# Performance work log

Hardware: AMD Instinct MI355X
Metric: run time of the kernel (lower is better)

## Reference

```python
import jax, jax.numpy as jnp
import numpy as np

DROPOUT = 0.5
ALPHA = 0.15
N_PROPAGATION = 5


def setup_inputs() -> dict:
    key = jax.random.key(0)
    k1, k2, k3, k4 = jax.random.split(key, 4)
    n_nodes, n_edges, d = 100000, 1600000, 48
    logits = jax.random.normal(k1, (n_nodes, d), dtype=jnp.float32)
    edge_val = jax.random.uniform(k2, (n_edges,), dtype=jnp.float32)
    edge_row = jax.random.randint(k3, (n_edges,), 0, n_nodes, dtype=jnp.int32)
    edge_col = jax.random.randint(k4, (n_edges,), 0, n_nodes, dtype=jnp.int32)
    return {"logits": logits, "edge_val": edge_val,
            "edge_row": edge_row, "edge_col": edge_col}


def reference(logits, edge_val, edge_row, edge_col):
    # APPNP-style power iteration: x <- (1-alpha) * dropout(A_hat) @ x + alpha * logits
    n_nodes = logits.shape[0]
    keep = 1.0 - DROPOUT
    drop_key = jax.random.key(42)
    a = logits
    x = logits
    for i in range(N_PROPAGATION):
        ki = jax.random.fold_in(drop_key, i)
        mask = jax.random.bernoulli(ki, keep, edge_val.shape)
        vals = jnp.where(mask, edge_val * (1.0 / keep), 0.0)  # inverted dropout on nnz values
        msg = vals[:, None] * x[edge_col]                      # [E, d] gather + scale
        spmm = jax.ops.segment_sum(msg, edge_row, num_segments=n_nodes)  # [N, d]
        x = (1.0 - ALPHA) * spmm + ALPHA * a
    return x
```

## Files before the change

### kernel.cpp

```cpp
#include <hip/hip_runtime.h>
#include <stdint.h>
#include <stddef.h>

#define D 48
#define BLK 256
#define BLKA 1024
#define EPTA 4
#define CHUNK (BLKA * EPTA)
#define BLD 512
#define BSH 9
#define NBKT_MAX 256
#define B97 0x30800000u

struct U2 { uint32_t a, b; };

__host__ __device__ constexpr U2 tf2x32(uint32_t k0, uint32_t k1, uint32_t c0, uint32_t c1) {
  uint32_t ks2 = k0 ^ k1 ^ 0x1BD11BDAu;
  uint32_t x0 = c0 + k0, x1 = c1 + k1;
#define TFR(r) x0 += x1; x1 = (x1 << (r)) | (x1 >> (32 - (r))); x1 ^= x0;
  TFR(13) TFR(15) TFR(26) TFR(6)
  x0 += k1; x1 += ks2 + 1u;
  TFR(17) TFR(29) TFR(16) TFR(24)
  x0 += ks2; x1 += k0 + 2u;
  TFR(13) TFR(15) TFR(26) TFR(6)
  x0 += k0; x1 += k1 + 3u;
  TFR(17) TFR(29) TFR(16) TFR(24)
  x0 += k1; x1 += ks2 + 4u;
  TFR(13) TFR(15) TFR(26) TFR(6)
  x0 += ks2; x1 += k0 + 5u;
#undef TFR
  return U2{x0, x1};
}

struct __align__(8) Edge { uint32_t cm; float val; };

__global__ __launch_bounds__(BLKA) void k_bkt_hist(
    const int* __restrict__ erow, int* __restrict__ bkt, int E, int nbkt) {
  __shared__ int h[NBKT_MAX];
  int t = threadIdx.x;
  int j0 = blockIdx.x * CHUNK;
  for (int i = t; i < nbkt; i += BLKA) h[i] = 0;
  __syncthreads();
#pragma unroll
  for (int k = 0; k < EPTA; ++k) {
    int j = j0 + k * BLKA + t;
    if (j < E) atomicAdd(&h[erow[j] >> BSH], 1);
  }
  __syncthreads();
  for (int i = t; i < nbkt; i += BLKA)
    if (h[i]) atomicAdd(&bkt[i], h[i]);
}

__global__ __launch_bounds__(BLK) void k_scan_bkt(
    int* __restrict__ bkt, int* __restrict__ bcur, int nbkt, int E) {
  __shared__ int s[BLK];
  int t = threadIdx.x;
  int v = (t < nbkt) ? bkt[t] : 0;
  s[t] = v;
  __syncthreads();
  for (int off = 1; off < BLK; off <<= 1) {
    int u = (t >= off) ? s[t - off] : 0;
    __syncthreads();
    s[t] += u;
    __syncthreads();
  }
  if (t < nbkt) {
    int excl = s[t] - v;
    bkt[t]  = excl;
    bcur[t] = excl;
  }
  if (t == 0) bkt[nbkt] = E;
}

__global__ __launch_bounds__(BLKA) void k_bucket_ms(
    const int* __restrict__ erow, const int* __restrict__ ecol,
    const float* __restrict__ eval,
    int* __restrict__ bcur, int* __restrict__ segcnt,
    Edge* __restrict__ es_b, int* __restrict__ rowb, int E, int nbkt) {
  __shared__ int h[NBKT_MAX];
  __shared__ int base[NBKT_MAX];
  __shared__ int hk[5][NBKT_MAX];
  constexpr U2 K0 = tf2x32(0u, 42u, 0u, 0u);
  constexpr U2 K1 = tf2x32(0u, 42u, 0u, 1u);
  constexpr U2 K2 = tf2x32(0u, 42u, 0u, 2u);
  constexpr U2 K3 = tf2x32(0u, 42u, 0u, 3u);
  constexpr U2 K4 = tf2x32(0u, 42u, 0u, 4u);
  int t = threadIdx.x;
  int j0 = blockIdx.x * CHUNK;
  for (int i = t; i < nbkt; i += BLKA) {
    h[i] = 0;
    for (int q = 0; q < 5; ++q) hk[q][i] = 0;
  }
  __syncthreads();
#pragma unroll
  for (int k = 0; k < EPTA; ++k) {
    int j = j0 + k * BLKA + t;
    if (j < E) atomicAdd(&h[erow[j] >> BSH], 1);
  }
  __syncthreads();
  for (int i = t; i < nbkt; i += BLKA)
    base[i] = h[i] ? atomicAdd(&bcur[i], h[i]) : 0;
  __syncthreads();
  for (int i = t; i < nbkt; i += BLKA) h[i] = 0;
  __syncthreads();
#pragma unroll
  for (int k = 0; k < EPTA; ++k) {
    int j = j0 + k * BLKA + t;
    if (j >= E) continue;
    int row = erow[j];
    int b = row >> BSH;
    uint32_t uj = (uint32_t)j;
    unsigned m = 0;
    U2 r;
    r = tf2x32(K0.a, K0.b, 0u, uj); m |= ((((r.a ^ r.b) >> 31) ^ 1u) << 0);
    r = tf2x32(K1.a, K1.b, 0u, uj); m |= ((((r.a ^ r.b) >> 31) ^ 1u) << 1);
    r = tf2x32(K2.a, K2.b, 0u, uj); m |= ((((r.a ^ r.b) >> 31) ^ 1u) << 2);
    r = tf2x32(K3.a, K3.b, 0u, uj); m |= ((((r.a ^ r.b) >> 31) ^ 1u) << 3);
    r = tf2x32(K4.a, K4.b, 0u, uj); m |= ((((r.a ^ r.b) >> 31) ^ 1u) << 4);
#pragma unroll
    for (int q = 0; q < 5; ++q)
      if ((m >> q) & 1u) atomicAdd(&hk[q][b], 1);
    int slot = atomicAdd(&h[b], 1);
    int p = base[b] + slot;
    Edge eg;
    eg.cm  = (uint32_t)ecol[j] | (m << 20);
    eg.val = eval[j] * 2.0f;
    es_b[p] = eg;
    rowb[p] = row;
  }
  __syncthreads();
  for (int i = t; i < nbkt; i += BLKA)
    for (int q = 0; q < 5; ++q)
      if (hk[q][i]) atomicAdd(&segcnt[q * nbkt + i], hk[q][i]);
}

__global__ __launch_bounds__(1024) void k_scan_seg(
    int* __restrict__ seg, int* __restrict__ rp5, int nbkt, int N) {
  __shared__ int s[1024];
  int t = threadIdx.x;
  int n = 5 * nbkt;
  int v = (t < n) ? seg[t] : 0;
  s[t] = v;
  __syncthreads();
  for (int off = 1; off < 1024; off <<= 1) {
    int u = (t >= off) ? s[t - off] : 0;
    __syncthreads();
    s[t] += u;
    __syncthreads();
  }
  if (t <= n) seg[t] = s[t] - v;
  __syncthreads();
  if (t < 5) rp5[(size_t)t * (N + 1) + N] = seg[(t + 1) * nbkt];
}

__global__ __launch_bounds__(BLD) void k_build(
    const Edge* __restrict__ es_b, const int* __restrict__ rowb,
    const int* __restrict__ bkt_off, const int* __restrict__ segoff,
    int* __restrict__ rp5, uint32_t* __restrict__ es_all, int N, int nbkt) {
  __shared__ int lc[5][1 << BSH];
  __shared__ int sc[1 << BSH];
  int b = blockIdx.x, t = threadIdx.x;
  int s = bkt_off[b], e = bkt_off[b + 1];
  int rbase = b << BSH;
#pragma unroll
  for (int i = 0; i < 5; ++i) lc[i][t] = 0;
  __syncthreads();
  for (int j = s + t; j < e; j += BLD) {
    int row = rowb[j] - rbase;
    unsigned m = es_b[j].cm >> 20;
#pragma unroll
    for (int i = 0; i < 5; ++i)
      if ((m >> i) & 1u) atomicAdd(&lc[i][row], 1);
  }
  __syncthreads();
  for (int i = 0; i < 5; ++i) {
    int v = lc[i][t];
    sc[t] = v;
    __syncthreads();
    for (int off = 1; off < BLD; off <<= 1) {
      int u = (t >= off) ? sc[t - off] : 0;
      __syncthreads();
      sc[t] += u;
      __syncthreads();
    }
    int pos = segoff[i * nbkt + b] + sc[t] - v;
    int row = rbase + t;
    if (row < N) rp5[(size_t)i * (N + 1) + row] = pos;
    lc[i][t] = pos;
    __syncthreads();
  }
  for (int j = s + t; j < e; j += BLD) {
    int row = rowb[j] - rbase;
    Edge eg = es_b[j];
    unsigned m = eg.cm >> 20;
    uint32_t vb = __float_as_uint(eg.val);
    uint32_t pk = (vb < B97) ? 0u : ((vb - B97 + (1u << 12)) >> 13);
    uint32_t entry = (eg.cm & 0x1FFFFu) | (pk << 17);
#pragma unroll
    for (int i = 0; i < 5; ++i)
      if ((m >> i) & 1u) {
        int p = atomicAdd(&lc[i][row], 1);
        es_all[p] = entry;
      }
  }
}

__global__ __launch_bounds__(BLK) void k_spmm(
    const int* __restrict__ rp, const uint32_t* __restrict__ es_all,
    const float* __restrict__ x, const float* __restrict__ logits,
    float* __restrict__ xn, int N) {
  int t = blockIdx.x * BLK + threadIdx.x;
  int r = t >> 4;
  if (r >= N) return;
  int sl = t & 15;
  int s = rp[r], e = rp[r + 1];
  float a0 = 0.f, a1 = 0.f, a2 = 0.f;
  const float* xb = x + 3 * sl;
  for (int k = s; k < e; k += 8) {
#pragma unroll
    for (int i = 0; i < 8; ++i) {
      int kk = k + i;
      bool in = kk < e;
      uint32_t u = es_all[kk];
      int c = in ? (int)(u & 0x1FFFFu) : 0;
      uint32_t vb = ((u >> 17) << 13) + B97;
      float v = in ? __uint_as_float(vb) : 0.0f;
      const float* xp = xb + (size_t)c * D;
      a0 = fmaf(v, xp[0], a0);
      a1 = fmaf(v, xp[1], a1);
      a2 = fmaf(v, xp[2], a2);
    }
  }
  size_t o = (size_t)r * D + 3 * sl;
  xn[o + 0] = 0.85f * a0 + 0.15f * logits[o + 0];
  xn[o + 1] = 0.85f * a1 + 0.15f * logits[o + 1];
  xn[o + 2] = 0.85f * a2 + 0.15f * logits[o + 2];
}

extern "C" void kernel_launch(void* const* d_in, const int* in_sizes, int n_in,
                              void* d_out, int out_size, void* d_ws, size_t ws_size,
                              hipStream_t stream) {
  const float* logits   = (const float*)d_in[0];
  const float* edge_val = (const float*)d_in[1];
  const int*   edge_row = (const int*)d_in[2];
  const int*   edge_col = (const int*)d_in[3];
  float* out = (float*)d_out;

  const int E = in_sizes[1];
  const int N = in_sizes[0] / D;
  const int EBC  = (E + CHUNK - 1) / CHUNK;
  const int NBKT = (N + (1 << BSH) - 1) >> BSH;

  char* p = (char*)d_ws;
  auto alloc = [&](size_t bytes) {
    char* q = p;
    p += (bytes + 255) & ~(size_t)255;
    return q;
  };
  int* rp5     = (int*)alloc((size_t)5 * (N + 1) * 4);
  int* bkt     = (int*)alloc((size_t)(NBKT + 1) * 4);
  int* bcur    = (int*)alloc((size_t)NBKT * 4);
  int* segcnt  = (int*)alloc((size_t)(5 * NBKT + 1) * 4);
  uint32_t* es_all = (uint32_t*)alloc(((size_t)E * 5 / 2 + 65536) * 4);
  size_t un_sz = (size_t)E * 12 + 512;
  size_t xa_sz = (size_t)N * D * 4;
  char* un = alloc(un_sz > xa_sz ? un_sz : xa_sz);
  Edge* es_b = (Edge*)un;
  int*  rowb = (int*)(un + (((size_t)E * 8 + 255) & ~(size_t)255));
  float* xA  = (float*)un;

  hipMemsetAsync(bkt, 0, (size_t)(NBKT + 1) * 4, stream);
  hipMemsetAsync(segcnt, 0, (size_t)(5 * NBKT + 1) * 4, stream);
  k_bkt_hist<<<EBC, BLKA, 0, stream>>>(edge_row, bkt, E, NBKT);
  k_scan_bkt<<<1, BLK, 0, stream>>>(bkt, bcur, NBKT, E);
  k_bucket_ms<<<EBC, BLKA, 0, stream>>>(edge_row, edge_col, edge_val,
                                        bcur, segcnt, es_b, rowb, E, NBKT);
  k_scan_seg<<<1, 1024, 0, stream>>>(segcnt, rp5, NBKT, N);
  k_build<<<NBKT, BLD, 0, stream>>>(es_b, rowb, bkt, segcnt, rp5, es_all, N, NBKT);

  const int RPB = BLK / 16;
  const float* src = logits;
  float* dst = out;
  for (int i = 0; i < 5; ++i) {
    k_spmm<<<(N + RPB - 1) / RPB, BLK, 0, stream>>>(rp5 + (size_t)i * (N + 1),
                                                    es_all, src, logits, dst, N);
    src = dst;
    dst = (dst == out) ? xA : out;
  }
}
```

Baseline: 330.9 us.

## Store propagated features and logits in bf16, halve lanes per row

The node feature matrix and logits are converted to bf16 with round-to-nearest-even. Each SpMM iteration then gathers packed bf16 pairs, accumulates in fp32 with 8 lanes per row handling 6 features each, and writes bf16 except on the final pass, which writes fp32. This halves the gather and store traffic in the propagation loop. Separately, the per-iteration dropout count histogram moves into the first histogram pass, so the bucketing kernel no longer does those atomics. The cost is bf16 rounding error compounded over five iterations, plus the mask being computed twice across the two passes.

```diff
diff --git a/kernel.cpp b/kernel.cpp
--- a/kernel.cpp
+++ b/kernel.cpp
@@ -32,23 +32,70 @@
   return U2{x0, x1};
 }
 
+__device__ __forceinline__ unsigned mask5_of(uint32_t uj) {
+  constexpr U2 K0 = tf2x32(0u, 42u, 0u, 0u);
+  constexpr U2 K1 = tf2x32(0u, 42u, 0u, 1u);
+  constexpr U2 K2 = tf2x32(0u, 42u, 0u, 2u);
+  constexpr U2 K3 = tf2x32(0u, 42u, 0u, 3u);
+  constexpr U2 K4 = tf2x32(0u, 42u, 0u, 4u);
+  unsigned m = 0;
+  U2 r;
+  r = tf2x32(K0.a, K0.b, 0u, uj); m |= ((((r.a ^ r.b) >> 31) ^ 1u) << 0);
+  r = tf2x32(K1.a, K1.b, 0u, uj); m |= ((((r.a ^ r.b) >> 31) ^ 1u) << 1);
+  r = tf2x32(K2.a, K2.b, 0u, uj); m |= ((((r.a ^ r.b) >> 31) ^ 1u) << 2);
+  r = tf2x32(K3.a, K3.b, 0u, uj); m |= ((((r.a ^ r.b) >> 31) ^ 1u) << 3);
+  r = tf2x32(K4.a, K4.b, 0u, uj); m |= ((((r.a ^ r.b) >> 31) ^ 1u) << 4);
+  return m;
+}
+
+__device__ __forceinline__ uint32_t rne16(float f) {
+  uint32_t u = __float_as_uint(f);
+  return (u + 0x7FFFu + ((u >> 16) & 1u)) >> 16;
+}
+__device__ __forceinline__ uint32_t pk2(float a, float b) {
+  return rne16(a) | (rne16(b) << 16);
+}
+
 struct __align__(8) Edge { uint32_t cm; float val; };
 
+__global__ __launch_bounds__(BLK) void k_prep(
+    const float4* __restrict__ in, uint2* __restrict__ outp, int n4) {
+  int i = blockIdx.x * BLK + threadIdx.x;
+  if (i >= n4) return;
+  float4 f = in[i];
+  outp[i] = make_uint2(pk2(f.x, f.y), pk2(f.z, f.w));
+}
+
 __global__ __launch_bounds__(BLKA) void k_bkt_hist(
-    const int* __restrict__ erow, int* __restrict__ bkt, int E, int nbkt) {
+    const int* __restrict__ erow, int* __restrict__ bkt,
+    int* __restrict__ segcnt, int E, int nbkt) {
   __shared__ int h[NBKT_MAX];
+  __shared__ int hk[5][NBKT_MAX + 1];
   int t = threadIdx.x;
   int j0 = blockIdx.x * CHUNK;
-  for (int i = t; i < nbkt; i += BLKA) h[i] = 0;
+  for (int i = t; i < nbkt; i += BLKA) {
+    h[i] = 0;
+    for (int q = 0; q < 5; ++q) hk[q][i] = 0;
+  }
   __syncthreads();
 #pragma unroll
   for (int k = 0; k < EPTA; ++k) {
     int j = j0 + k * BLKA + t;
-    if (j < E) atomicAdd(&h[erow[j] >> BSH], 1);
-  }
-  __syncthreads();
-  for (int i = t; i < nbkt; i += BLKA)
+    if (j < E) {
+      int b = erow[j] >> BSH;
+      atomicAdd(&h[b], 1);
+      unsigned m = mask5_of((uint32_t)j);
+#pragma unroll
+      for (int q = 0; q < 5; ++q)
+        if ((m >> q) & 1u) atomicAdd(&hk[q][b], 1);
+    }
+  }
+  __syncthreads();
+  for (int i = t; i < nbkt; i += BLKA) {
     if (h[i]) atomicAdd(&bkt[i], h[i]);
+    for (int q = 0; q < 5; ++q)
+      if (hk[q][i]) atomicAdd(&segcnt[q * nbkt + i], hk[q][i]);
+  }
 }
 
 __global__ __launch_bounds__(BLK) void k_scan_bkt(
@@ -75,22 +122,13 @@
 __global__ __launch_bounds__(BLKA) void k_bucket_ms(
     const int* __restrict__ erow, const int* __restrict__ ecol,
     const float* __restrict__ eval,
-    int* __restrict__ bcur, int* __restrict__ segcnt,
-    Edge* __restrict__ es_b, int* __restrict__ rowb, int E, int nbkt) {
+    int* __restrict__ bcur, Edge* __restrict__ es_b, int* __restrict__ rowb,
+    int E, int nbkt) {
   __shared__ int h[NBKT_MAX];
   __shared__ int base[NBKT_MAX];
-  __shared__ int hk[5][NBKT_MAX];
-  constexpr U2 K0 = tf2x32(0u, 42u, 0u, 0u);
-  constexpr U2 K1 = tf2x32(0u, 42u, 0u, 1u);
-  constexpr U2 K2 = tf2x32(0u, 42u, 0u, 2u);
-  constexpr U2 K3 = tf2x32(0u, 42u, 0u, 3u);
-  constexpr U2 K4 = tf2x32(0u, 42u, 0u, 4u);
   int t = threadIdx.x;
   int j0 = blockIdx.x * CHUNK;
-  for (int i = t; i < nbkt; i += BLKA) {
-    h[i] = 0;
-    for (int q = 0; q < 5; ++q) hk[q][i] = 0;
-  }
+  for (int i = t; i < nbkt; i += BLKA) h[i] = 0;
   __syncthreads();
 #pragma unroll
   for (int k = 0; k < EPTA; ++k) {
@@ -109,17 +147,7 @@
     if (j >= E) continue;
     int row = erow[j];
     int b = row >> BSH;
-    uint32_t uj = (uint32_t)j;
-    unsigned m = 0;
-    U2 r;
-    r = tf2x32(K0.a, K0.b, 0u, uj); m |= ((((r.a ^ r.b) >> 31) ^ 1u) << 0);
-    r = tf2x32(K1.a, K1.b, 0u, uj); m |= ((((r.a ^ r.b) >> 31) ^ 1u) << 1);
-    r = tf2x32(K2.a, K2.b, 0u, uj); m |= ((((r.a ^ r.b) >> 31) ^ 1u) << 2);
-    r = tf2x32(K3.a, K3.b, 0u, uj); m |= ((((r.a ^ r.b) >> 31) ^ 1u) << 3);
-    r = tf2x32(K4.a, K4.b, 0u, uj); m |= ((((r.a ^ r.b) >> 31) ^ 1u) << 4);
-#pragma unroll
-    for (int q = 0; q < 5; ++q)
-      if ((m >> q) & 1u) atomicAdd(&hk[q][b], 1);
+    unsigned m = mask5_of((uint32_t)j);
     int slot = atomicAdd(&h[b], 1);
     int p = base[b] + slot;
     Edge eg;
@@ -128,10 +156,6 @@
     es_b[p] = eg;
     rowb[p] = row;
   }
-  __syncthreads();
-  for (int i = t; i < nbkt; i += BLKA)
-    for (int q = 0; q < 5; ++q)
-      if (hk[q][i]) atomicAdd(&segcnt[q * nbkt + i], hk[q][i]);
 }
 
 __global__ __launch_bounds__(1024) void k_scan_seg(
@@ -205,17 +229,18 @@
   }
 }
 
-__global__ __launch_bounds__(BLK) void k_spmm(
+template<int FINAL>
+__global__ __launch_bounds__(BLK) void k_spmm_b(
     const int* __restrict__ rp, const uint32_t* __restrict__ es_all,
-    const float* __restrict__ x, const float* __restrict__ logits,
-    float* __restrict__ xn, int N) {
+    const uint32_t* __restrict__ xs, const uint32_t* __restrict__ lb,
+    uint32_t* __restrict__ xd, float* __restrict__ xf, int N) {
   int t = blockIdx.x * BLK + threadIdx.x;
-  int r = t >> 4;
+  int r = t >> 3;
   if (r >= N) return;
-  int sl = t & 15;
+  int sl = t & 7;
   int s = rp[r], e = rp[r + 1];
-  float a0 = 0.f, a1 = 0.f, a2 = 0.f;
-  const float* xb = x + 3 * sl;
+  float a0 = 0.f, a1 = 0.f, a2 = 0.f, a3 = 0.f, a4 = 0.f, a5 = 0.f;
+  const uint32_t* xb = xs + 3 * sl;
   for (int k = s; k < e; k += 8) {
 #pragma unroll
     for (int i = 0; i < 8; ++i) {
@@ -225,16 +250,33 @@
       int c = in ? (int)(u & 0x1FFFFu) : 0;
       uint32_t vb = ((u >> 17) << 13) + B97;
       float v = in ? __uint_as_float(vb) : 0.0f;
-      const float* xp = xb + (size_t)c * D;
-      a0 = fmaf(v, xp[0], a0);
-      a1 = fmaf(v, xp[1], a1);
-      a2 = fmaf(v, xp[2], a2);
+      const uint32_t* xp = xb + (size_t)c * 24;
+      uint32_t u0 = xp[0], u1 = xp[1], u2 = xp[2];
+      a0 = fmaf(v, __uint_as_float(u0 << 16), a0);
+      a1 = fmaf(v, __uint_as_float(u0 & 0xFFFF0000u), a1);
+      a2 = fmaf(v, __uint_as_float(u1 << 16), a2);
+      a3 = fmaf(v, __uint_as_float(u1 & 0xFFFF0000u), a3);
+      a4 = fmaf(v, __uint_as_float(u2 << 16), a4);
+      a5 = fmaf(v, __uint_as_float(u2 & 0xFFFF0000u), a5);
     }
   }
-  size_t o = (size_t)r * D + 3 * sl;
-  xn[o + 0] = 0.85f * a0 + 0.15f * logits[o + 0];
-  xn[o + 1] = 0.85f * a1 + 0.15f * logits[o + 1];
-  xn[o + 2] = 0.85f * a2 + 0.15f * logits[o + 2];
+  int base = r * 24 + 3 * sl;
+  uint32_t l0 = lb[base], l1 = lb[base + 1], l2 = lb[base + 2];
+  float o0 = 0.85f * a0 + 0.15f * __uint_as_float(l0 << 16);
+  float o1 = 0.85f * a1 + 0.15f * __uint_as_float(l0 & 0xFFFF0000u);
+  float o2 = 0.85f * a2 + 0.15f * __uint_as_float(l1 << 16);
+  float o3 = 0.85f * a3 + 0.15f * __uint_as_float(l1 & 0xFFFF0000u);
+  float o4 = 0.85f * a4 + 0.15f * __uint_as_float(l2 << 16);
+  float o5 = 0.85f * a5 + 0.15f * __uint_as_float(l2 & 0xFFFF0000u);
+  if (FINAL) {
+    size_t ob = (size_t)r * D + 6 * sl;
+    xf[ob + 0] = o0; xf[ob + 1] = o1; xf[ob + 2] = o2;
+    xf[ob + 3] = o3; xf[ob + 4] = o4; xf[ob + 5] = o5;
+  } else {
+    xd[base]     = pk2(o0, o1);
+    xd[base + 1] = pk2(o2, o3);
+    xd[base + 2] = pk2(o4, o5);
+  }
 }
 
 extern "C" void kernel_launch(void* const* d_in, const int* in_sizes, int n_in,
@@ -262,29 +304,31 @@
   int* bcur    = (int*)alloc((size_t)NBKT * 4);
   int* segcnt  = (int*)alloc((size_t)(5 * NBKT + 1) * 4);
   uint32_t* es_all = (uint32_t*)alloc(((size_t)E * 5 / 2 + 65536) * 4);
+  uint32_t* lb     = (uint32_t*)alloc((size_t)N * D * 2);
   size_t un_sz = (size_t)E * 12 + 512;
-  size_t xa_sz = (size_t)N * D * 4;
-  char* un = alloc(un_sz > xa_sz ? un_sz : xa_sz);
+  size_t xx_sz = (size_t)N * D * 4 + 512;
+  char* un = alloc(un_sz > xx_sz ? un_sz : xx_sz);
   Edge* es_b = (Edge*)un;
   int*  rowb = (int*)(un + (((size_t)E * 8 + 255) & ~(size_t)255));
-  float* xA  = (float*)un;
+  uint32_t* xb0 = (uint32_t*)un;
+  uint32_t* xb1 = (uint32_t*)(un + (((size_t)N * D * 2 + 255) & ~(size_t)255));
 
   hipMemsetAsync(bkt, 0, (size_t)(NBKT + 1) * 4, stream);
   hipMemsetAsync(segcnt, 0, (size_t)(5 * NBKT + 1) * 4, stream);
-  k_bkt_hist<<<EBC, BLKA, 0, stream>>>(edge_row, bkt, E, NBKT);
+  k_prep<<<(N * D / 4 + BLK - 1) / BLK, BLK, 0, stream>>>(
+      (const float4*)logits, (uint2*)lb, N * D / 4);
+  k_bkt_hist<<<EBC, BLKA, 0, stream>>>(edge_row, bkt, segcnt, E, NBKT);
   k_scan_bkt<<<1, BLK, 0, stream>>>(bkt, bcur, NBKT, E);
   k_bucket_ms<<<EBC, BLKA, 0, stream>>>(edge_row, edge_col, edge_val,
-                                        bcur, segcnt, es_b, rowb, E, NBKT);
+                                        bcur, es_b, rowb, E, NBKT);
   k_scan_seg<<<1, 1024, 0, stream>>>(segcnt, rp5, NBKT, N);
   k_build<<<NBKT, BLD, 0, stream>>>(es_b, rowb, bkt, segcnt, rp5, es_all, N, NBKT);
 
-  const int RPB = BLK / 16;
-  const float* src = logits;
-  float* dst = out;
-  for (int i = 0; i < 5; ++i) {
-    k_spmm<<<(N + RPB - 1) / RPB, BLK, 0, stream>>>(rp5 + (size_t)i * (N + 1),
-                                                    es_all, src, logits, dst, N);
-    src = dst;
-    dst = (dst == out) ? xA : out;
-  }
-}
+  const int RPB = BLK / 8;
+  const int GB  = (N + RPB - 1) / RPB;
+  k_spmm_b<0><<<GB, BLK, 0, stream>>>(rp5 + 0 * (size_t)(N + 1), es_all, lb, lb, xb0, nullptr, N);
+  k_spmm_b<0><<<GB, BLK, 0, stream>>>(rp5 + 1 * (size_t)(N + 1), es_all, xb0, lb, xb1, nullptr, N);
+  k_spmm_b<0><<<GB, BLK, 0, stream>>>(rp5 + 2 * (size_t)(N + 1), es_all, xb1, lb, xb0, nullptr, N);
+  k_spmm_b<0><<<GB, BLK, 0, stream>>>(rp5 + 3 * (size_t)(N + 1), es_all, xb0, lb, xb1, nullptr, N);
+  k_spmm_b<1><<<GB, BLK, 0, stream>>>(rp5 + 4 * (size_t)(N + 1), es_all, xb1, lb, nullptr, out, N);
+}
```

New measurement: 308.3 us. 1.07x faster.
